# Performance work log

Hardware: AMD Instinct MI355X
Metric: run time of the kernel (lower is better)

## Reference

```python
import jax, jax.numpy as jnp
import numpy as np

FEATURE_IN = 4096
FEATURE_OUT = 4096
R = 16
ALPHA = 32.0


def setup_inputs() -> dict:
    key = jax.random.key(0)
    k_x, k_w, k_b, k_a = jax.random.split(key, 4)
    x = jax.random.normal(k_x, (4, 2048, FEATURE_IN), dtype=jnp.float32)
    # base linear (torch nn.Linear): weight [out, in], bias [out]
    bound = 1.0 / np.sqrt(FEATURE_IN)
    w = jax.random.uniform(k_w, (FEATURE_OUT, FEATURE_IN), dtype=jnp.float32, minval=-bound, maxval=bound)
    b = jax.random.uniform(k_b, (FEATURE_OUT,), dtype=jnp.float32, minval=-bound, maxval=bound)
    # lora_a: kaiming uniform over [feature_in, r]; lora_b: zeros -> use small randn so grads are nontrivial? No: faithful init is zeros, but zeros makes LoRA path trivially zero. Use kaiming for a, small random for b to exercise the math.
    gain = np.sqrt(2.0 / (1.0 + 5.0 ** 2))  # kaiming_uniform default a=sqrt(5)
    bound_a = gain * np.sqrt(3.0 / FEATURE_IN)
    lora_a = jax.random.uniform(k_a, (FEATURE_IN, R), dtype=jnp.float32, minval=-bound_a, maxval=bound_a)
    lora_b = jax.random.normal(jax.random.fold_in(key, 7), (R, FEATURE_OUT), dtype=jnp.float32) * 0.01
    return {"x": x, "w": w, "b": b, "lora_a": lora_a, "lora_b": lora_b}


def reference(x, w, b, lora_a, lora_b):
    # base linear: x @ W^T + b
    output1 = jnp.einsum('bsi,oi->bso', x, w) + b
    # faithful to source: materialize (A @ B) [feature_in, feature_out] first,
    # then x @ (A@B), scaled by alpha/r
    ab = jnp.matmul(lora_a, lora_b)  # [feature_in, feature_out]
    output2 = jnp.matmul(x, ab) * (ALPHA / R)
    return output2 + output1
```

## Files before the change

kernel.cpp:

```cpp
#include <hip/hip_runtime.h>
#include <cstdint>
#include <cstddef>

#define FEATURE_IN 4096
#define FEATURE_OUT 4096
#define RNK 16

typedef __bf16 bf16x8_t __attribute__((ext_vector_type(8)));
typedef __bf16 bf16x4_t __attribute__((ext_vector_type(4)));
typedef float f32x4_t __attribute__((ext_vector_type(4)));

#define FW_KB 128
#define FW_NB 32
#define NFUSE 4096
#define NCVTB 2048
#define CVT_THREADS (NCVTB * 256)
#define CVT_CHUNKS 16

__global__ __launch_bounds__(256) void prep_all(const float* __restrict__ x,
                                                uint16_t* __restrict__ xb,
                                                const float* __restrict__ w,
                                                const float* __restrict__ la,
                                                const float* __restrict__ lb,
                                                uint16_t* __restrict__ wf) {
    __shared__ float las[FW_KB * RNK];
    __shared__ float lbs[RNK * FW_NB];

    const int tid = threadIdx.x;

    if (blockIdx.x >= NFUSE) {
        const int tg = (blockIdx.x - NFUSE) * 256 + tid;
        const f32x4_t* xp = (const f32x4_t*)x;
        bf16x4_t* op = (bf16x4_t*)xb;
#pragma unroll
        for (int i = 0; i < CVT_CHUNKS; ++i) {
            const int idx = i * CVT_THREADS + tg;
            f32x4_t v = xp[idx];
            bf16x4_t o;
            o[0] = (__bf16)v[0]; o[1] = (__bf16)v[1];
            o[2] = (__bf16)v[2]; o[3] = (__bf16)v[3];
            op[idx] = o;
        }
        return;
    }

    const int bid = blockIdx.x;
    const int kb = (bid & 31) * FW_KB;
    const int nb = (bid >> 5) * FW_NB;

    {
        const float4* src = (const float4*)(la + (size_t)kb * RNK);
        float4* dst = (float4*)las;
        dst[tid] = src[tid];
        dst[tid + 256] = src[tid + 256];
    }
#pragma unroll
    for (int f = tid; f < RNK * FW_NB; f += 256) {
        int r = f >> 5;
        int nl = f & 31;
        lbs[r * FW_NB + nl] = lb[(size_t)r * FEATURE_OUT + nb + nl];
    }
    __syncthreads();

    const int nl = tid >> 3;
    const int kq = tid & 7;

    f32x4_t bcol[4];
#pragma unroll
    for (int r4 = 0; r4 < 4; ++r4) {
        f32x4_t v;
#pragma unroll
        for (int j = 0; j < 4; ++j) v[j] = lbs[(r4 * 4 + j) * FW_NB + nl];
        bcol[r4] = v;
    }

    const f32x4_t* las4 = (const f32x4_t*)las;
    const float* wrow = w + (size_t)(nb + nl) * FEATURE_IN + kb + kq * 16;
    uint16_t* wfrow = wf + (size_t)(nb + nl) * FEATURE_IN + kb + kq * 16;

#pragma unroll
    for (int h = 0; h < 2; ++h) {
        float4 wv0 = ((const float4*)wrow)[h * 2 + 0];
        float4 wv1 = ((const float4*)wrow)[h * 2 + 1];
        float wfv[8] = {wv0.x, wv0.y, wv0.z, wv0.w, wv1.x, wv1.y, wv1.z, wv1.w};
        bf16x8_t o;
#pragma unroll
        for (int j = 0; j < 8; ++j) {
            const int k = kq * 16 + h * 8 + j;
            float s = 0.f;
#pragma unroll
            for (int rr = 0; rr < 4; ++rr) {
                const int r4 = (rr + kq) & 3;
                f32x4_t av = las4[k * 4 + r4];
                f32x4_t bv = bcol[r4];
                s += av[0] * bv[0] + av[1] * bv[1] + av[2] * bv[2] + av[3] * bv[3];
            }
            o[j] = (__bf16)(wfv[j] + 2.f * s);
        }
        ((bf16x8_t*)wfrow)[h] = o;
    }
}

#define BM 256
#define BN 256
#define BK 32
#define NT (FEATURE_IN / BK)

#define ABUF(b) ((b) * 32768)
#define BBUF(b) ((b) * 32768 + 16384)

#define MFMA16X(S) do { _Pragma("unroll")                                                \
    for (int _mi = 0; _mi < 4; ++_mi) { _Pragma("unroll")                                \
        for (int _ni = 0; _ni < 4; ++_ni)                                                \
            acc[_mi][_ni] = __builtin_amdgcn_mfma_f32_16x16x32_bf16(                     \
                afx[_mi], bqr[S][_ni], acc[_mi][_ni], 0, 0, 0); } } while (0)

#define MFMA16Y(S) do { _Pragma("unroll")                                                \
    for (int _mi = 0; _mi < 4; ++_mi) { _Pragma("unroll")                                \
        for (int _ni = 0; _ni < 4; ++_ni)                                                \
            acc[4 + _mi][_ni] = __builtin_amdgcn_mfma_f32_16x16x32_bf16(                 \
                afy[_mi], bqr[S][_ni], acc[4 + _mi][_ni], 0, 0, 0); } } while (0)

#define READ_AFY(b) do { _Pragma("unroll")                                               \
    for (int _mi = 0; _mi < 4; ++_mi)                                                    \
        afy[_mi] = *(const bf16x8_t*)(lds + ABUF(b) + aoff[4 + _mi]); } while (0)

#define READ_R0(b, SN) do { _Pragma("unroll")                                            \
    for (int _mi = 0; _mi < 4; ++_mi)                                                    \
        afx[_mi] = *(const bf16x8_t*)(lds + ABUF(b) + aoff[_mi]);                        \
    _Pragma("unroll")                                                                    \
    for (int _ni = 0; _ni < 4; ++_ni)                                                    \
        bqr[SN][_ni] = *(const bf16x8_t*)(lds + BBUF(b) + boff[_ni]); } while (0)

#define GLL(SRC, DSTOFF)                                                                 \
    __builtin_amdgcn_global_load_lds(                                                    \
        (const __attribute__((address_space(1))) void*)(SRC),                            \
        (__attribute__((address_space(3))) void*)(lds + (DSTOFF) + wv * 1024), 16, 0, 0)

#define STAGE_AB(b) do {                                                                 \
    GLL(pA0, ABUF(b)); GLL(pA1, ABUF(b) + 8192);                                         \
    GLL(pB0, BBUF(b)); GLL(pB1, BBUF(b) + 8192);                                         \
    pA0 += BK; pA1 += BK; pB0 += BK; pB1 += BK; } while (0)

#define PBAR() __builtin_amdgcn_s_barrier()
#define PRIO1 __builtin_amdgcn_s_setprio(1)
#define PRIO0 __builtin_amdgcn_s_setprio(0)
#define VMCNT(n) asm volatile("s_waitcnt vmcnt(" #n ")" ::: "memory")
#define LGKM0() asm volatile("s_waitcnt lgkmcnt(0)" ::: "memory")
#define SCHEDB() __builtin_amdgcn_sched_barrier(0)

#define BODY(B, S)                                                                       \
    READ_AFY(B);                                                                         \
    SCHEDB();                                                                            \
    PRIO1; MFMA16X(S); PRIO0;                                                            \
    VMCNT(4);                                                                            \
    LGKM0();                                                                             \
    PBAR();                                                                              \
    STAGE_AB((B + 3) & 3);                                                               \
    READ_R0((B + 1) & 3, (S) ^ 1);                                                       \
    SCHEDB();                                                                            \
    PRIO1; MFMA16Y(S); PRIO0;

#define TAILB(B, S, NWAIT)                                                               \
    READ_AFY(B);                                                                         \
    SCHEDB();                                                                            \
    PRIO1; MFMA16X(S); PRIO0;                                                            \
    VMCNT(NWAIT);                                                                        \
    LGKM0();                                                                             \
    PBAR();                                                                              \
    READ_R0((B + 1) & 3, (S) ^ 1);                                                       \
    SCHEDB();                                                                            \
    PRIO1; MFMA16Y(S); PRIO0;

__global__ __launch_bounds__(512, 2) void gemm256(const uint16_t* __restrict__ Au,
                                                  const uint16_t* __restrict__ Bu,
                                                  const float* __restrict__ bias,
                                                  float* __restrict__ C,
                                                  int M, int N, int K) {
    __shared__ __align__(16) char lds[131072];

    const __bf16* A = (const __bf16*)Au;
    const __bf16* B = (const __bf16*)Bu;

    const int tid  = threadIdx.x;
    const int wv   = tid >> 6;
    const int lane = tid & 63;
    const int waveM = wv >> 2;
    const int waveN = wv & 3;
    const int l15 = lane & 15;
    const int q   = lane >> 4;

    const int nbx = N / BN;
    const int nwg = nbx * (M / BM);
    const int bidlin = blockIdx.y * nbx + blockIdx.x;
    const int swz = (bidlin & 7) * (nwg >> 3) + (bidlin >> 3);
    const int by = swz / nbx;
    const int bx = swz - by * nbx;
    const int m0 = by * BM;
    const int n0 = bx * BN;

    const int srow = tid >> 2;
    const int sq   = ((tid & 3) - (srow >> 1)) & 3;
    const __bf16* pA0 = A + (size_t)(m0 + srow) * K + sq * 8;
    const __bf16* pA1 = pA0 + (size_t)128 * K;
    const __bf16* pB0 = B + (size_t)(n0 + srow) * K + sq * 8;
    const __bf16* pB1 = pB0 + (size_t)128 * K;

    int aoff[8], boff[4];
#pragma unroll
    for (int mi = 0; mi < 8; ++mi) {
        int row = waveM * 128 + mi * 16 + l15;
        aoff[mi] = row * 64 + (((row >> 1) + q) & 3) * 16;
    }
#pragma unroll
    for (int ni = 0; ni < 4; ++ni) {
        int row = waveN * 64 + ni * 16 + l15;
        boff[ni] = row * 64 + (((row >> 1) + q) & 3) * 16;
    }

    f32x4_t acc[8][4];
#pragma unroll
    for (int mi = 0; mi < 8; ++mi)
#pragma unroll
        for (int ni = 0; ni < 4; ++ni)
            acc[mi][ni] = (f32x4_t)0.f;

    bf16x8_t afx[4], afy[4], bqr[2][4];

    STAGE_AB(0);
    STAGE_AB(1);
    STAGE_AB(2);
    VMCNT(8);
    PBAR();
    READ_R0(0, 0);

#pragma unroll 1
    for (int i = 0; i < 31; ++i) {
        BODY(0, 0)
        BODY(1, 1)
        BODY(2, 0)
        BODY(3, 1)
    }
    BODY(0, 0)

    TAILB(1, 1, 4)
    TAILB(2, 0, 0)
    READ_AFY(3);
    SCHEDB();
    PRIO1; MFMA16X(1); PRIO0;
    PRIO1; MFMA16Y(1); PRIO0;

#pragma unroll
    for (int ni = 0; ni < 4; ++ni) {
        const int col = n0 + waveN * 64 + ni * 16 + l15;
        const float bv = bias[col];
#pragma unroll
        for (int mi = 0; mi < 8; ++mi) {
            const int row = m0 + waveM * 128 + mi * 16 + q * 4;
            float* op = C + (size_t)row * N + col;
#pragma unroll
            for (int j = 0; j < 4; ++j)
                op[(size_t)j * N] = acc[mi][ni][j] + bv;
        }
    }
}

extern "C" void kernel_launch(void* const* d_in, const int* in_sizes, int n_in,
                              void* d_out, int out_size, void* d_ws, size_t ws_size,
                              hipStream_t stream) {
    const float* x  = (const float*)d_in[0];
    const float* w  = (const float*)d_in[1];
    const float* b  = (const float*)d_in[2];
    const float* la = (const float*)d_in[3];
    const float* lb = (const float*)d_in[4];
    float* out = (float*)d_out;

    const int M = in_sizes[0] / FEATURE_IN;
    const int K = FEATURE_IN;
    const int N = FEATURE_OUT;

    uint16_t* xb = (uint16_t*)d_ws;
    uint16_t* wf = (uint16_t*)((char*)d_ws + (size_t)M * K * 2);

    prep_all<<<NFUSE + NCVTB, 256, 0, stream>>>(x, xb, w, la, lb, wf);

    {
        dim3 grid(N / BN, M / BM);
        gemm256<<<grid, 512, 0, stream>>>(xb, wf, b, out, M, N, K);
    }
}
```

Before: 512.9 us.

## Load B fragments directly from global into registers, halve LDS staging

The GEMM no longer stages the B (weight) tile through LDS. Each wave now loads its own B fragments straight from global memory into registers one step ahead, so only A is staged via global_load_lds, which halves LDS use and LDS read traffic. A second barrier is added per half-step, the vmcnt accounting is reworked, and the block-index swizzle is replaced with a simpler grouping. The trade-off is that B is now read redundantly across the two M-waves with less coalesced access, and the extra barriers add synchronisation cost.

```diff
diff --git a/kernel.cpp b/kernel.cpp
--- a/kernel.cpp
+++ b/kernel.cpp
@@ -9,6 +9,8 @@
 typedef __bf16 bf16x8_t __attribute__((ext_vector_type(8)));
 typedef __bf16 bf16x4_t __attribute__((ext_vector_type(4)));
 typedef float f32x4_t __attribute__((ext_vector_type(4)));
+
+typedef const __attribute__((address_space(1))) bf16x8_t* gb8p;
 
 #define FW_KB 128
 #define FW_NB 32
@@ -106,8 +108,7 @@
 #define BK 32
 #define NT (FEATURE_IN / BK)
 
-#define ABUF(b) ((b) * 32768)
-#define BBUF(b) ((b) * 32768 + 16384)
+#define ABUF(b) ((b) * 16384)
 
 #define MFMA16X(S) do { _Pragma("unroll")                                                \
     for (int _mi = 0; _mi < 4; ++_mi) { _Pragma("unroll")                                \
@@ -125,59 +126,61 @@
     for (int _mi = 0; _mi < 4; ++_mi)                                                    \
         afy[_mi] = *(const bf16x8_t*)(lds + ABUF(b) + aoff[4 + _mi]); } while (0)
 
-#define READ_R0(b, SN) do { _Pragma("unroll")                                            \
+#define READ_R0A(b) do { _Pragma("unroll")                                               \
     for (int _mi = 0; _mi < 4; ++_mi)                                                    \
-        afx[_mi] = *(const bf16x8_t*)(lds + ABUF(b) + aoff[_mi]);                        \
-    _Pragma("unroll")                                                                    \
-    for (int _ni = 0; _ni < 4; ++_ni)                                                    \
-        bqr[SN][_ni] = *(const bf16x8_t*)(lds + BBUF(b) + boff[_ni]); } while (0)
+        afx[_mi] = *(const bf16x8_t*)(lds + ABUF(b) + aoff[_mi]); } while (0)
 
 #define GLL(SRC, DSTOFF)                                                                 \
     __builtin_amdgcn_global_load_lds(                                                    \
         (const __attribute__((address_space(1))) void*)(SRC),                            \
         (__attribute__((address_space(3))) void*)(lds + (DSTOFF) + wv * 1024), 16, 0, 0)
 
-#define STAGE_AB(b) do {                                                                 \
-    GLL(pA0, ABUF(b)); GLL(pA1, ABUF(b) + 8192);                                         \
-    GLL(pB0, BBUF(b)); GLL(pB1, BBUF(b) + 8192);                                         \
-    pA0 += BK; pA1 += BK; pB0 += BK; pB1 += BK; } while (0)
+#define STAGE_A(b) do { GLL(pA0, ABUF(b)); GLL(pA1, ABUF(b) + 8192);                     \
+                        pA0 += BK; pA1 += BK; } while (0)
+
+#define BQLOAD(SN) do {                                                                  \
+    bqr[SN][0] = *(gb8p)(pBq0); pBq0 += BK;                                              \
+    bqr[SN][1] = *(gb8p)(pBq1); pBq1 += BK;                                              \
+    bqr[SN][2] = *(gb8p)(pBq2); pBq2 += BK;                                              \
+    bqr[SN][3] = *(gb8p)(pBq3); pBq3 += BK; } while (0)
 
 #define PBAR() __builtin_amdgcn_s_barrier()
 #define PRIO1 __builtin_amdgcn_s_setprio(1)
 #define PRIO0 __builtin_amdgcn_s_setprio(0)
 #define VMCNT(n) asm volatile("s_waitcnt vmcnt(" #n ")" ::: "memory")
-#define LGKM0() asm volatile("s_waitcnt lgkmcnt(0)" ::: "memory")
 #define SCHEDB() __builtin_amdgcn_sched_barrier(0)
 
 #define BODY(B, S)                                                                       \
     READ_AFY(B);                                                                         \
+    STAGE_A((B + 3) & 3);                                                                \
+    BQLOAD((S) ^ 1);                                                                     \
+    VMCNT(6);                                                                            \
     SCHEDB();                                                                            \
     PRIO1; MFMA16X(S); PRIO0;                                                            \
-    VMCNT(4);                                                                            \
-    LGKM0();                                                                             \
     PBAR();                                                                              \
-    STAGE_AB((B + 3) & 3);                                                               \
-    READ_R0((B + 1) & 3, (S) ^ 1);                                                       \
-    SCHEDB();                                                                            \
-    PRIO1; MFMA16Y(S); PRIO0;
+    READ_R0A((B + 1) & 3);                                                               \
+    SCHEDB();                                                                            \
+    PRIO1; MFMA16Y(S); PRIO0;                                                            \
+    PBAR();
 
 #define TAILB(B, S, NWAIT)                                                               \
     READ_AFY(B);                                                                         \
+    BQLOAD((S) ^ 1);                                                                     \
+    VMCNT(NWAIT);                                                                        \
     SCHEDB();                                                                            \
     PRIO1; MFMA16X(S); PRIO0;                                                            \
-    VMCNT(NWAIT);                                                                        \
-    LGKM0();                                                                             \
     PBAR();                                                                              \
-    READ_R0((B + 1) & 3, (S) ^ 1);                                                       \
-    SCHEDB();                                                                            \
-    PRIO1; MFMA16Y(S); PRIO0;
+    READ_R0A((B + 1) & 3);                                                               \
+    SCHEDB();                                                                            \
+    PRIO1; MFMA16Y(S); PRIO0;                                                            \
+    PBAR();
 
 __global__ __launch_bounds__(512, 2) void gemm256(const uint16_t* __restrict__ Au,
                                                   const uint16_t* __restrict__ Bu,
                                                   const float* __restrict__ bias,
                                                   float* __restrict__ C,
                                                   int M, int N, int K) {
-    __shared__ __align__(16) char lds[131072];
+    __shared__ __align__(16) char lds[65536];
 
     const __bf16* A = (const __bf16*)Au;
     const __bf16* B = (const __bf16*)Bu;
@@ -191,11 +194,9 @@
     const int q   = lane >> 4;
 
     const int nbx = N / BN;
-    const int nwg = nbx * (M / BM);
     const int bidlin = blockIdx.y * nbx + blockIdx.x;
-    const int swz = (bidlin & 7) * (nwg >> 3) + (bidlin >> 3);
-    const int by = swz / nbx;
-    const int bx = swz - by * nbx;
+    const int bx = (bidlin & 7) * 2 + ((bidlin >> 3) & 1);
+    const int by = bidlin >> 4;
     const int m0 = by * BM;
     const int n0 = bx * BN;
 
@@ -203,20 +204,18 @@
     const int sq   = ((tid & 3) - (srow >> 1)) & 3;
     const __bf16* pA0 = A + (size_t)(m0 + srow) * K + sq * 8;
     const __bf16* pA1 = pA0 + (size_t)128 * K;
-    const __bf16* pB0 = B + (size_t)(n0 + srow) * K + sq * 8;
-    const __bf16* pB1 = pB0 + (size_t)128 * K;
-
-    int aoff[8], boff[4];
+
+    const __bf16* pBq0 = B + (size_t)(n0 + waveN * 64 + 0  + l15) * K + q * 8;
+    const __bf16* pBq1 = B + (size_t)(n0 + waveN * 64 + 16 + l15) * K + q * 8;
+    const __bf16* pBq2 = B + (size_t)(n0 + waveN * 64 + 32 + l15) * K + q * 8;
+    const __bf16* pBq3 = B + (size_t)(n0 + waveN * 64 + 48 + l15) * K + q * 8;
+
+    int aoff[8];
 #pragma unroll
     for (int mi = 0; mi < 8; ++mi) {
         int row = waveM * 128 + mi * 16 + l15;
         aoff[mi] = row * 64 + (((row >> 1) + q) & 3) * 16;
     }
-#pragma unroll
-    for (int ni = 0; ni < 4; ++ni) {
-        int row = waveN * 64 + ni * 16 + l15;
-        boff[ni] = row * 64 + (((row >> 1) + q) & 3) * 16;
-    }
 
     f32x4_t acc[8][4];
 #pragma unroll
@@ -227,12 +226,13 @@
 
     bf16x8_t afx[4], afy[4], bqr[2][4];
 
-    STAGE_AB(0);
-    STAGE_AB(1);
-    STAGE_AB(2);
+    STAGE_A(0);
+    STAGE_A(1);
+    STAGE_A(2);
+    BQLOAD(0);
     VMCNT(8);
     PBAR();
-    READ_R0(0, 0);
+    READ_R0A(0);
 
 #pragma unroll 1
     for (int i = 0; i < 31; ++i) {
@@ -244,8 +244,9 @@
     BODY(0, 0)
 
     TAILB(1, 1, 4)
-    TAILB(2, 0, 0)
+    TAILB(2, 0, 4)
     READ_AFY(3);
+    VMCNT(0);
     SCHEDB();
     PRIO1; MFMA16X(1); PRIO0;
     PRIO1; MFMA16Y(1); PRIO0;
```

Result: slower. 657.4 us (+28.2%).
